# Kernel tuning notes

Measured on AMD Instinct MI355X. Metric: run time of the kernel, lower is better.

## Reference

```python
import jax, jax.numpy as jnp
import numpy as np

B, N, M, D, H = 4, 2048, 2048, 1024, 16
HD = D // H


def setup_inputs() -> dict:
    key = jax.random.key(0)
    ks = jax.random.split(key, 16)
    s = 1.0 / np.sqrt(D)
    inp = {
        "Q": jax.random.normal(ks[0], (B, N, D), jnp.float32),
        "K": jax.random.normal(ks[1], (B, M, D), jnp.float32),
        "V": jax.random.normal(ks[2], (B, M, D), jnp.float32),
        "attn_bias": jax.random.normal(ks[3], (B, N, M), jnp.float32),
        "mask": jax.random.randint(ks[4], (B, M), 0, 2).astype(bool),
        # linear params (torch nn.Linear: y = x @ W.T + b)
        "Wq": jax.random.uniform(ks[5], (D, D), jnp.float32, -s, s),
        "bq": jax.random.uniform(ks[6], (D,), jnp.float32, -s, s),
        "Wk": jax.random.uniform(ks[7], (D, D), jnp.float32, -s, s),
        "bk": jax.random.uniform(ks[8], (D,), jnp.float32, -s, s),
        "Wv": jax.random.uniform(ks[9], (D, D), jnp.float32, -s, s),
        "bv": jax.random.uniform(ks[10], (D,), jnp.float32, -s, s),
        "Wo": jax.random.uniform(ks[11], (D, D), jnp.float32, -s, s),
        "bo": jax.random.uniform(ks[12], (D,), jnp.float32, -s, s),
    }
    return inp


def reference(Q, K, V, attn_bias, mask, Wq, bq, Wk, bk, Wv, bv, Wo, bo):
    b, n, d = Q.shape
    m = K.shape[1]
    # bias (B,N,M) -> (B,1,N,M); mask (B,M) True = masked out (-inf)
    bias = attn_bias[:, None, :, :]
    bias = jnp.where(mask[:, None, None, :], -jnp.inf, bias)
    # projections, split heads: (B, H, len, head_dim)
    q = (Q @ Wq.T + bq).reshape(b, n, H, HD).transpose(0, 2, 1, 3)
    k = (K @ Wk.T + bk).reshape(b, m, H, HD).transpose(0, 2, 1, 3)
    v = (V @ Wv.T + bv).reshape(b, m, H, HD).transpose(0, 2, 1, 3)
    scale = 1.0 / np.sqrt(HD).astype(np.float32)
    attn = jnp.einsum("bhid,bhjd->bhij", q * scale, k) + bias
    attn = jax.nn.softmax(attn, axis=-1)
    out = jnp.einsum("bhij,bhjd->bhid", attn, v)
    out = out.transpose(0, 2, 1, 3).reshape(b, n, d)
    return out @ Wo.T + bo
```

## Files before the change

kernel.cpp:

```cpp
#include <hip/hip_runtime.h>
#include <hip/hip_bf16.h>

#define Bq 4
#define Nq 2048
#define Mq 2048
#define Dq 1024
#define Hq 16

typedef __attribute__((ext_vector_type(8))) short short8;
typedef __attribute__((ext_vector_type(4))) short short4v;
typedef __attribute__((ext_vector_type(4))) float floatx4;
typedef __attribute__((ext_vector_type(16))) float floatx16;
typedef __attribute__((ext_vector_type(4))) unsigned uint4v;

static __device__ __forceinline__ short f2bf(float f) {
    __hip_bfloat16 h = __float2bfloat16(f);
    short r;
    __builtin_memcpy(&r, &h, 2);
    return r;
}
static __device__ __forceinline__ float bf2f(short s) {
    unsigned u = ((unsigned)(unsigned short)s) << 16;
    float f;
    __builtin_memcpy(&f, &u, 4);
    return f;
}
static __device__ __forceinline__ unsigned cvtpk_bf16(float lo, float hi) {
    unsigned r;
    asm("v_cvt_pk_bf16_f32 %0, %1, %2" : "=v"(r) : "v"(lo), "v"(hi));
    return r;
}
static __device__ __forceinline__ void swap32(unsigned &a, unsigned &b) {
    asm("v_permlane32_swap_b32 %0, %1" : "+v"(a), "+v"(b));
}
static __device__ __forceinline__ float exp2_fast(float x) {
    float r;
    asm("v_exp_f32 %0, %1" : "=v"(r) : "v"(x));
    return r;
}
static __device__ __forceinline__ void gld16(const void* g, void* l) {
    __builtin_amdgcn_global_load_lds(
        (const __attribute__((address_space(1))) unsigned int*)g,
        (__attribute__((address_space(3))) unsigned int*)l, 16, 0, 0);
}

__global__ void bias_prep(const float* __restrict__ bias, const int* __restrict__ mask,
                          short* __restrict__ out)
{
    const long i = ((long)blockIdx.x * 256 + threadIdx.x) * 8;
    const int m = (int)(i & (Mq - 1));
    const int b = (int)(i >> 22);
    floatx4 f0 = *(const floatx4*)(bias + i);
    floatx4 f1 = *(const floatx4*)(bias + i + 4);
    const int* mp = mask + b * Mq + m;
    short8 o;
#pragma unroll
    for (int e = 0; e < 4; ++e) {
        o[e]     = mp[e]     ? f2bf(-1e38f) : f2bf(f0[e] * 1.44269504f);
        o[e + 4] = mp[e + 4] ? f2bf(-1e38f) : f2bf(f1[e] * 1.44269504f);
    }
    *(short8*)(out + i) = o;
}

__global__ void cvt_w(const float* __restrict__ w0, const float* __restrict__ w1,
                      const float* __restrict__ w2, const float* __restrict__ w3,
                      short* __restrict__ out)
{
    const int z = blockIdx.y;
    const float* s = (z == 0) ? w0 : (z == 1) ? w1 : (z == 2) ? w2 : w3;
    short* d = out + (size_t)z * (Dq * Dq);
    const int i = (blockIdx.x * 256 + threadIdx.x) * 8;
    floatx4 f0 = *(const floatx4*)(s + i);
    floatx4 f1 = *(const floatx4*)(s + i + 4);
    short8 o;
#pragma unroll
    for (int e = 0; e < 4; ++e) { o[e] = f2bf(f0[e]); o[e + 4] = f2bf(f1[e]); }
    *(short8*)(d + i) = o;
}

struct GB {
    const void* A[3];
    const short* W[3];
    const float* bias[3];
    void* C[3];
    float scale[3];
    int omode[3];
};

template<bool ABF>
__global__ __launch_bounds__(256, 3)
void gemm_bt(GB gb, int K)
{
    __shared__ __align__(16) short As[2][128 * 32];
    __shared__ __align__(16) short Bs[2][128 * 32];

    const int z = blockIdx.z;
    const char* Ap = (const char*)gb.A[z];
    const short* Wp = gb.W[z];

    const int tid = threadIdx.x;
    const int lane = tid & 63;
    const int wid = tid >> 6;
    const int wr = wid >> 1, wc = wid & 1;
    const int g = lane >> 4, c = lane & 15;
    const long row0 = (long)blockIdx.x * 128;
    const int col0 = blockIdx.y * 128;

    const int srow = tid >> 1;
    const int sk = (tid & 1) * 16;
    const int R0 = tid >> 2;
    const int ub = (tid & 3) ^ ((R0 >> 1) & 3);
    const short* bsrc = Wp + ((long)col0 + R0) * K + ub * 8;

    floatx4 acc[4][4];
#pragma unroll
    for (int i = 0; i < 4; ++i)
#pragma unroll
        for (int j = 0; j < 4; ++j) acc[i][j] = (floatx4)0.0f;

    {
        char* d0 = (char*)Bs + wid * 1024;
        gld16(bsrc, d0);
        gld16(bsrc + 64L * K, d0 + 4096);
    }
    {
        short8 a0, a1;
        if constexpr (ABF) {
            const short* ap = (const short*)Ap + (row0 + srow) * (long)K + sk;
            a0 = *(const short8*)ap; a1 = *(const short8*)(ap + 8);
        } else {
            const float* ap = (const float*)Ap + (row0 + srow) * (long)K + sk;
            floatx4 f0 = *(const floatx4*)ap,       f1 = *(const floatx4*)(ap + 4),
                    f2 = *(const floatx4*)(ap + 8), f3 = *(const floatx4*)(ap + 12);
#pragma unroll
            for (int e = 0; e < 4; ++e) {
                a0[e] = f2bf(f0[e]); a0[e + 4] = f2bf(f1[e]);
                a1[e] = f2bf(f2[e]); a1[e + 4] = f2bf(f3[e]);
            }
        }
        short8* As8 = (short8*)As;
        const int u0 = sk >> 3, sw = (srow >> 1) & 3;
        As8[srow * 4 + ((u0)     ^ sw)] = a0;
        As8[srow * 4 + ((u0 + 1) ^ sw)] = a1;
    }
    __syncthreads();

    int buf = 0;
    for (int kt = 0; kt < K; kt += 32) {
        const bool nlast = (kt + 32 < K);
        floatx4 f0, f1, f2, f3;
        short8 s0, s1;
        if (nlast) {
            char* d0 = (char*)Bs + (buf ^ 1) * 8192 + wid * 1024;
            gld16(bsrc + kt + 32, d0);
            gld16(bsrc + 64L * K + kt + 32, d0 + 4096);
            if constexpr (ABF) {
                const short* ap = (const short*)Ap + (row0 + srow) * (long)K + kt + 32 + sk;
                s0 = *(const short8*)ap; s1 = *(const short8*)(ap + 8);
            } else {
                const float* ap = (const float*)Ap + (row0 + srow) * (long)K + kt + 32 + sk;
                f0 = *(const floatx4*)ap;       f1 = *(const floatx4*)(ap + 4);
                f2 = *(const floatx4*)(ap + 8); f3 = *(const floatx4*)(ap + 12);
            }
        }
        short8* As8 = (short8*)((char*)As + buf * 8192);
        short8* Bs8 = (short8*)((char*)Bs + buf * 8192);
        short8 af[4], bfq[4];
#pragma unroll
        for (int fm = 0; fm < 4; ++fm) {
            const int r = wr * 64 + fm * 16 + c;
            af[fm] = As8[r * 4 + (g ^ ((r >> 1) & 3))];
        }
#pragma unroll
        for (int fn = 0; fn < 4; ++fn) {
            const int cc = wc * 64 + fn * 16 + c;
            bfq[fn] = Bs8[cc * 4 + (g ^ ((cc >> 1) & 3))];
        }
#pragma unroll
        for (int fm = 0; fm < 4; ++fm)
#pragma unroll
            for (int fn = 0; fn < 4; ++fn)
                acc[fm][fn] = __builtin_amdgcn_mfma_f32_16x16x32_bf16(af[fm], bfq[fn], acc[fm][fn], 0, 0, 0);
        if (nlast) {
            short8 a0, a1;
            if constexpr (ABF) { a0 = s0; a1 = s1; }
            else {
#pragma unroll
                for (int e = 0; e < 4; ++e) {
                    a0[e] = f2bf(f0[e]); a0[e + 4] = f2bf(f1[e]);
                    a1[e] = f2bf(f2[e]); a1[e + 4] = f2bf(f3[e]);
                }
            }
            short8* An8 = (short8*)((char*)As + (buf ^ 1) * 8192);
            const int u0 = sk >> 3, sw = (srow >> 1) & 3;
            An8[srow * 4 + ((u0)     ^ sw)] = a0;
            An8[srow * 4 + ((u0 + 1) ^ sw)] = a1;
        }
        __syncthreads();
        buf ^= 1;
    }

    const float sc = gb.scale[z];
    const float* bp = gb.bias[z];
    const int om = gb.omode[z];
    void* Cp = gb.C[z];
#pragma unroll
    for (int fn = 0; fn < 4; ++fn) {
        const int ccol = col0 + wc * 64 + fn * 16 + c;
        const float bv = bp[ccol];
#pragma unroll
        for (int fm = 0; fm < 4; ++fm) {
            const long r0 = row0 + wr * 64 + fm * 16 + g * 4;
#pragma unroll
            for (int reg = 0; reg < 4; ++reg) {
                const float val = (acc[fm][fn][reg] + bv) * sc;
                const long rr = r0 + reg;
                if (om == 0) {
                    ((short*)Cp)[rr * Dq + ccol] = f2bf(val);
                } else if (om == 1) {
                    const long idx = ((long)(rr >> 11) * Dq + ccol) * (long)Mq + (rr & (Mq - 1));
                    ((short*)Cp)[idx] = f2bf(val);
                } else {
                    ((float*)Cp)[rr * Dq + ccol] = val;
                }
            }
        }
    }
}

__global__ __launch_bounds__(256, 4)
void attn_fused(const short* __restrict__ qg_, const short* __restrict__ kg_,
                const short* __restrict__ vtg, const short* __restrict__ bmg,
                short* __restrict__ outg)
{
    __shared__ __align__(16) short k_lds[2][64 * 64];
    __shared__ __align__(16) short v_lds[2][64 * 64];

    const int tid = threadIdx.x;
    const int lane = tid & 63;
    const int w = tid >> 6;
    const int hi = lane >> 5;
    const int q31 = lane & 31;

    const int blk = blockIdx.x;
    const int bh = blk & 63;
    const int qt = blk >> 6;
    const int b = bh >> 4, h = bh & 15;

    const long qbase = (long)b * Nq + qt * 128 + w * 32;

    short8 qf[4];
#pragma unroll
    for (int ks = 0; ks < 4; ++ks)
        qf[ks] = *(const short8*)(qg_ + (qbase + q31) * Dq + h * 64 + ks * 16 + hi * 8);

    floatx16 oa[2];
    oa[0] = (floatx16)0.0f; oa[1] = (floatx16)0.0f;
    float m_s = -1e37f, l_s = 0.0f;

    const int sr = tid >> 3;
    const int su = (tid & 7) ^ (sr & 7);
    const char* ksrc = (const char*)(kg_ + ((long)b * Mq + sr) * Dq + h * 64 + su * 8);
    const char* vsrc = (const char*)(vtg + ((long)b * Dq + h * 64 + sr) * Mq + su * 8);

#define STAGE(bf, kt2) do {                                                   \
        const long j0b = (long)(kt2) * 64;                                    \
        char* kd = (char*)k_lds + (bf) * 8192 + w * 1024;                     \
        char* vd = (char*)v_lds + (bf) * 8192 + w * 1024;                     \
        gld16(ksrc + j0b * (Dq * 2), kd);                                     \
        gld16(ksrc + (j0b + 32) * (Dq * 2), kd + 4096);                       \
        gld16(vsrc + j0b * 2, vd);                                            \
        gld16(vsrc + 32L * Mq * 2 + j0b * 2, vd + 4096);                      \
    } while (0)

    STAGE(0, 0);
    __syncthreads();

    int buf = 0;
    for (int kt = 0; kt < 32; ++kt) {
        if (kt < 31) STAGE(buf ^ 1, kt + 1);
        const short* brow = bmg + (qbase + q31) * Mq + (long)kt * 64;
        short4v bb[8];
#pragma unroll
        for (int kg = 0; kg < 2; ++kg)
#pragma unroll
            for (int Qh = 0; Qh < 4; ++Qh)
                bb[kg * 4 + Qh] = *(const short4v*)(brow + kg * 32 + Qh * 8 + hi * 4);

        const char* kb = (const char*)k_lds + buf * 8192;
        const char* vb = (const char*)v_lds + buf * 8192;

        floatx16 sa[2];
#pragma unroll
        for (int kg = 0; kg < 2; ++kg) {
            short8 kf[4];
#pragma unroll
            for (int ks = 0; ks < 4; ++ks) {
                const int r = kg * 32 + q31;
                const int up = (2 * ks + hi) ^ (r & 7);
                kf[ks] = *(const short8*)(kb + r * 128 + up * 16);
            }
            sa[kg] = (floatx16)0.0f;
#pragma unroll
            for (int ks = 0; ks < 4; ++ks)
                sa[kg] = __builtin_amdgcn_mfma_f32_32x32x16_bf16(kf[ks], qf[ks], sa[kg], 0, 0, 0);
        }

        float p[32];
#pragma unroll
        for (int kg = 0; kg < 2; ++kg)
#pragma unroll
            for (int Qh = 0; Qh < 4; ++Qh) {
                const short4v bv4 = bb[kg * 4 + Qh];
#pragma unroll
                for (int e = 0; e < 4; ++e)
                    p[kg * 16 + Qh * 4 + e] = sa[kg][Qh * 4 + e] + bf2f(bv4[e]);
            }
        float t16[16];
#pragma unroll
        for (int i = 0; i < 16; ++i) t16[i] = fmaxf(p[2 * i], p[2 * i + 1]);
#pragma unroll
        for (int i = 0; i < 8; ++i) t16[i] = fmaxf(t16[2 * i], t16[2 * i + 1]);
        t16[0] = fmaxf(fmaxf(fmaxf(t16[0], t16[1]), fmaxf(t16[2], t16[3])),
                       fmaxf(fmaxf(t16[4], t16[5]), fmaxf(t16[6], t16[7])));
        const float pm = fmaxf(t16[0], __shfl_xor(t16[0], 32));
        if (!__all(pm <= m_s + 11.5f)) {
            const float mn = fmaxf(m_s, pm);
            const float al = exp2_fast(m_s - mn);
            l_s *= al;
            oa[0] *= al; oa[1] *= al;
            m_s = mn;
        }
#pragma unroll
        for (int i = 0; i < 32; ++i) p[i] = exp2_fast(p[i] - m_s);
        float s16[16];
#pragma unroll
        for (int i = 0; i < 16; ++i) s16[i] = p[2 * i] + p[2 * i + 1];
#pragma unroll
        for (int i = 0; i < 8; ++i) s16[i] = s16[2 * i] + s16[2 * i + 1];
        float rs = ((s16[0] + s16[1]) + (s16[2] + s16[3])) +
                   ((s16[4] + s16[5]) + (s16[6] + s16[7]));
        rs += __shfl_xor(rs, 32);
        l_s += rs;

        uint4v pw[4];
#pragma unroll
        for (int kg = 0; kg < 2; ++kg) {
            unsigned w0 = cvtpk_bf16(p[kg * 16 + 0], p[kg * 16 + 1]);
            unsigned w1 = cvtpk_bf16(p[kg * 16 + 2], p[kg * 16 + 3]);
            unsigned w2 = cvtpk_bf16(p[kg * 16 + 4], p[kg * 16 + 5]);
            unsigned w3 = cvtpk_bf16(p[kg * 16 + 6], p[kg * 16 + 7]);
            swap32(w0, w2); swap32(w1, w3);
            pw[kg * 2][0] = w0; pw[kg * 2][1] = w1; pw[kg * 2][2] = w2; pw[kg * 2][3] = w3;
            unsigned w4 = cvtpk_bf16(p[kg * 16 + 8],  p[kg * 16 + 9]);
            unsigned w5 = cvtpk_bf16(p[kg * 16 + 10], p[kg * 16 + 11]);
            unsigned w6 = cvtpk_bf16(p[kg * 16 + 12], p[kg * 16 + 13]);
            unsigned w7 = cvtpk_bf16(p[kg * 16 + 14], p[kg * 16 + 15]);
            swap32(w4, w6); swap32(w5, w7);
            pw[kg * 2 + 1][0] = w4; pw[kg * 2 + 1][1] = w5; pw[kg * 2 + 1][2] = w6; pw[kg * 2 + 1][3] = w7;
        }

#pragma unroll
        for (int dg = 0; dg < 2; ++dg) {
            short8 vf[4];
#pragma unroll
            for (int ks = 0; ks < 4; ++ks) {
                const int r = dg * 32 + q31;
                const int up = (2 * ks + hi) ^ (r & 7);
                vf[ks] = *(const short8*)(vb + r * 128 + up * 16);
            }
#pragma unroll
            for (int ks = 0; ks < 4; ++ks)
                oa[dg] = __builtin_amdgcn_mfma_f32_32x32x16_bf16(
                    vf[ks], __builtin_bit_cast(short8, pw[ks]), oa[dg], 0, 0, 0);
        }
        __syncthreads();
        buf ^= 1;
    }
#undef STAGE

    const float invl = 1.0f / l_s;
    short* op = outg + (qbase + q31) * Dq + h * 64;
#pragma unroll
    for (int dg = 0; dg < 2; ++dg)
#pragma unroll
        for (int Qh = 0; Qh < 4; ++Qh) {
            short4v t;
#pragma unroll
            for (int e = 0; e < 4; ++e)
                t[e] = f2bf(oa[dg][Qh * 4 + e] * invl);
            *(short4v*)(op + dg * 32 + Qh * 8 + hi * 4) = t;
        }
}

extern "C" void kernel_launch(void* const* d_in, const int* in_sizes, int n_in,
                              void* d_out, int out_size, void* d_ws, size_t ws_size,
                              hipStream_t stream)
{
    const float* Q    = (const float*)d_in[0];
    const float* K    = (const float*)d_in[1];
    const float* V    = (const float*)d_in[2];
    const float* bias = (const float*)d_in[3];
    const int*   mask = (const int*)d_in[4];
    const float* Wq   = (const float*)d_in[5];
    const float* bq   = (const float*)d_in[6];
    const float* Wk   = (const float*)d_in[7];
    const float* bk   = (const float*)d_in[8];
    const float* Wv   = (const float*)d_in[9];
    const float* bv   = (const float*)d_in[10];
    const float* Wo   = (const float*)d_in[11];
    const float* bo   = (const float*)d_in[12];

    const size_t TSZ = (size_t)Bq * Nq * Dq;
    short* q_ws  = (short*)d_ws;
    short* k_ws  = q_ws  + TSZ;
    short* vt_ws = k_ws  + TSZ;
    short* a_ws  = vt_ws + TSZ;
    short* bm_ws = a_ws  + TSZ;
    short* w_ws  = bm_ws + (size_t)Bq * Nq * Mq;
    (void)ws_size;

    bias_prep<<<dim3(8192), dim3(256), 0, stream>>>(bias, mask, bm_ws);
    cvt_w<<<dim3(512, 4), dim3(256), 0, stream>>>(Wq, Wk, Wv, Wo, w_ws);

    GB g1{};
    g1.A[0] = Q;  g1.A[1] = K;  g1.A[2] = V;
    g1.W[0] = w_ws; g1.W[1] = w_ws + Dq * Dq; g1.W[2] = w_ws + 2 * Dq * Dq;
    g1.bias[0] = bq; g1.bias[1] = bk; g1.bias[2] = bv;
    g1.C[0] = q_ws; g1.C[1] = k_ws; g1.C[2] = vt_ws;
    g1.scale[0] = 0.125f * 1.44269504f; g1.scale[1] = 1.0f; g1.scale[2] = 1.0f;
    g1.omode[0] = 0; g1.omode[1] = 0; g1.omode[2] = 1;
    gemm_bt<false><<<dim3(64, 8, 3), dim3(256), 0, stream>>>(g1, Dq);

    attn_fused<<<dim3(1024), dim3(256), 0, stream>>>(q_ws, k_ws, vt_ws, bm_ws, a_ws);

    GB g2{};
    g2.A[0] = a_ws;
    g2.W[0] = w_ws + 3 * Dq * Dq;
    g2.bias[0] = bo;
    g2.C[0] = d_out;
    g2.scale[0] = 1.0f;
    g2.omode[0] = 2;
    gemm_bt<true><<<dim3(64, 8, 1), dim3(256), 0, stream>>>(g2, Dq);
}
```

Measured before the change: 342.4 us.

## Pre-convert QKV inputs to bf16 and stage A via direct LDS loads

Adds a conversion pass that turns Q, K and V into bf16 in aliased workspace buffers, so the projection gemm can load both operands with direct global-to-LDS copies instead of converting fp32 in registers. bias_prep is moved after the projection to reuse the workspace. The attention kernel also initialises the score accumulator with the bias so the MFMA performs the add. This costs an extra full read and write of the inputs in exchange for a simpler, better-pipelined gemm loop.

```diff
diff --git a/kernel.cpp b/kernel.cpp
--- a/kernel.cpp
+++ b/kernel.cpp
@@ -62,14 +62,14 @@
     *(short8*)(out + i) = o;
 }
 
-__global__ void cvt_w(const float* __restrict__ w0, const float* __restrict__ w1,
-                      const float* __restrict__ w2, const float* __restrict__ w3,
-                      short* __restrict__ out)
+__global__ void cvt_bf(const float* __restrict__ s0, const float* __restrict__ s1,
+                       const float* __restrict__ s2, const float* __restrict__ s3,
+                       short* __restrict__ out, long per)
 {
     const int z = blockIdx.y;
-    const float* s = (z == 0) ? w0 : (z == 1) ? w1 : (z == 2) ? w2 : w3;
-    short* d = out + (size_t)z * (Dq * Dq);
-    const int i = (blockIdx.x * 256 + threadIdx.x) * 8;
+    const float* s = (z == 0) ? s0 : (z == 1) ? s1 : (z == 2) ? s2 : s3;
+    short* d = out + (long)z * per;
+    const long i = ((long)blockIdx.x * 256 + threadIdx.x) * 8;
     floatx4 f0 = *(const floatx4*)(s + i);
     floatx4 f1 = *(const floatx4*)(s + i + 4);
     short8 o;
@@ -79,7 +79,7 @@
 }
 
 struct GB {
-    const void* A[3];
+    const short* A[3];
     const short* W[3];
     const float* bias[3];
     void* C[3];
@@ -87,15 +87,14 @@
     int omode[3];
 };
 
-template<bool ABF>
 __global__ __launch_bounds__(256, 3)
-void gemm_bt(GB gb, int K)
+void gemm_all(GB gb, int K)
 {
     __shared__ __align__(16) short As[2][128 * 32];
     __shared__ __align__(16) short Bs[2][128 * 32];
 
     const int z = blockIdx.z;
-    const char* Ap = (const char*)gb.A[z];
+    const short* Ap = gb.A[z];
     const short* Wp = gb.W[z];
 
     const int tid = threadIdx.x;
@@ -106,10 +105,9 @@
     const long row0 = (long)blockIdx.x * 128;
     const int col0 = blockIdx.y * 128;
 
-    const int srow = tid >> 1;
-    const int sk = (tid & 1) * 16;
     const int R0 = tid >> 2;
     const int ub = (tid & 3) ^ ((R0 >> 1) & 3);
+    const short* asrc = Ap + (row0 + R0) * (long)K + ub * 8;
     const short* bsrc = Wp + ((long)col0 + R0) * K + ub * 8;
 
     floatx4 acc[4][4];
@@ -118,51 +116,21 @@
 #pragma unroll
         for (int j = 0; j < 4; ++j) acc[i][j] = (floatx4)0.0f;
 
-    {
-        char* d0 = (char*)Bs + wid * 1024;
-        gld16(bsrc, d0);
-        gld16(bsrc + 64L * K, d0 + 4096);
-    }
-    {
-        short8 a0, a1;
-        if constexpr (ABF) {
-            const short* ap = (const short*)Ap + (row0 + srow) * (long)K + sk;
-            a0 = *(const short8*)ap; a1 = *(const short8*)(ap + 8);
-        } else {
-            const float* ap = (const float*)Ap + (row0 + srow) * (long)K + sk;
-            floatx4 f0 = *(const floatx4*)ap,       f1 = *(const floatx4*)(ap + 4),
-                    f2 = *(const floatx4*)(ap + 8), f3 = *(const floatx4*)(ap + 12);
-#pragma unroll
-            for (int e = 0; e < 4; ++e) {
-                a0[e] = f2bf(f0[e]); a0[e + 4] = f2bf(f1[e]);
-                a1[e] = f2bf(f2[e]); a1[e + 4] = f2bf(f3[e]);
-            }
-        }
-        short8* As8 = (short8*)As;
-        const int u0 = sk >> 3, sw = (srow >> 1) & 3;
-        As8[srow * 4 + ((u0)     ^ sw)] = a0;
-        As8[srow * 4 + ((u0 + 1) ^ sw)] = a1;
-    }
+#define GSTAGE(buf, koff) do {                                                \
+        char* ad = (char*)As + (buf) * 8192 + wid * 1024;                     \
+        char* bd = (char*)Bs + (buf) * 8192 + wid * 1024;                     \
+        gld16(asrc + (koff), ad);                                             \
+        gld16(asrc + 64L * K + (koff), ad + 4096);                            \
+        gld16(bsrc + (koff), bd);                                             \
+        gld16(bsrc + 64L * K + (koff), bd + 4096);                            \
+    } while (0)
+
+    GSTAGE(0, 0);
     __syncthreads();
 
     int buf = 0;
     for (int kt = 0; kt < K; kt += 32) {
-        const bool nlast = (kt + 32 < K);
-        floatx4 f0, f1, f2, f3;
-        short8 s0, s1;
-        if (nlast) {
-            char* d0 = (char*)Bs + (buf ^ 1) * 8192 + wid * 1024;
-            gld16(bsrc + kt + 32, d0);
-            gld16(bsrc + 64L * K + kt + 32, d0 + 4096);
-            if constexpr (ABF) {
-                const short* ap = (const short*)Ap + (row0 + srow) * (long)K + kt + 32 + sk;
-                s0 = *(const short8*)ap; s1 = *(const short8*)(ap + 8);
-            } else {
-                const float* ap = (const float*)Ap + (row0 + srow) * (long)K + kt + 32 + sk;
-                f0 = *(const floatx4*)ap;       f1 = *(const floatx4*)(ap + 4);
-                f2 = *(const floatx4*)(ap + 8); f3 = *(const floatx4*)(ap + 12);
-            }
-        }
+        if (kt + 32 < K) GSTAGE(buf ^ 1, kt + 32);
         short8* As8 = (short8*)((char*)As + buf * 8192);
         short8* Bs8 = (short8*)((char*)Bs + buf * 8192);
         short8 af[4], bfq[4];
@@ -181,24 +149,10 @@
 #pragma unroll
             for (int fn = 0; fn < 4; ++fn)
                 acc[fm][fn] = __builtin_amdgcn_mfma_f32_16x16x32_bf16(af[fm], bfq[fn], acc[fm][fn], 0, 0, 0);
-        if (nlast) {
-            short8 a0, a1;
-            if constexpr (ABF) { a0 = s0; a1 = s1; }
-            else {
-#pragma unroll
-                for (int e = 0; e < 4; ++e) {
-                    a0[e] = f2bf(f0[e]); a0[e + 4] = f2bf(f1[e]);
-                    a1[e] = f2bf(f2[e]); a1[e + 4] = f2bf(f3[e]);
-                }
-            }
-            short8* An8 = (short8*)((char*)As + (buf ^ 1) * 8192);
-            const int u0 = sk >> 3, sw = (srow >> 1) & 3;
-            An8[srow * 4 + ((u0)     ^ sw)] = a0;
-            An8[srow * 4 + ((u0 + 1) ^ sw)] = a1;
-        }
         __syncthreads();
         buf ^= 1;
     }
+#undef GSTAGE
 
     const float sc = gb.scale[z];
     const float* bp = gb.bias[z];
@@ -292,6 +246,15 @@
 
         floatx16 sa[2];
 #pragma unroll
+        for (int kg = 0; kg < 2; ++kg)
+#pragma unroll
+            for (int Qh = 0; Qh < 4; ++Qh) {
+                const short4v b4 = bb[kg * 4 + Qh];
+#pragma unroll
+                for (int e = 0; e < 4; ++e)
+                    sa[kg][Qh * 4 + e] = bf2f(b4[e]);
+            }
+#pragma unroll
         for (int kg = 0; kg < 2; ++kg) {
             short8 kf[4];
 #pragma unroll
@@ -300,7 +263,6 @@
                 const int up = (2 * ks + hi) ^ (r & 7);
                 kf[ks] = *(const short8*)(kb + r * 128 + up * 16);
             }
-            sa[kg] = (floatx16)0.0f;
 #pragma unroll
             for (int ks = 0; ks < 4; ++ks)
                 sa[kg] = __builtin_amdgcn_mfma_f32_32x32x16_bf16(kf[ks], qf[ks], sa[kg], 0, 0, 0);
@@ -310,12 +272,8 @@
 #pragma unroll
         for (int kg = 0; kg < 2; ++kg)
 #pragma unroll
-            for (int Qh = 0; Qh < 4; ++Qh) {
-                const short4v bv4 = bb[kg * 4 + Qh];
-#pragma unroll
-                for (int e = 0; e < 4; ++e)
-                    p[kg * 16 + Qh * 4 + e] = sa[kg][Qh * 4 + e] + bf2f(bv4[e]);
-            }
+            for (int j = 0; j < 16; ++j)
+                p[kg * 16 + j] = sa[kg][j];
         float t16[16];
 #pragma unroll
         for (int i = 0; i < 16; ++i) t16[i] = fmaxf(p[2 * i], p[2 * i + 1]);
@@ -417,20 +375,25 @@
     short* vt_ws = k_ws  + TSZ;
     short* a_ws  = vt_ws + TSZ;
     short* bm_ws = a_ws  + TSZ;
-    short* w_ws  = bm_ws + (size_t)Bq * Nq * Mq;
+    short* w_ws  = bm_ws + 2 * TSZ;
+    short* qin_ws = a_ws;
+    short* kin_ws = bm_ws;
+    short* vin_ws = bm_ws + TSZ;
     (void)ws_size;
 
-    bias_prep<<<dim3(8192), dim3(256), 0, stream>>>(bias, mask, bm_ws);
-    cvt_w<<<dim3(512, 4), dim3(256), 0, stream>>>(Wq, Wk, Wv, Wo, w_ws);
+    cvt_bf<<<dim3(512, 4), dim3(256), 0, stream>>>(Wq, Wk, Wv, Wo, w_ws, (long)Dq * Dq);
+    cvt_bf<<<dim3(4096, 3), dim3(256), 0, stream>>>(Q, K, V, V, qin_ws, (long)TSZ);
 
     GB g1{};
-    g1.A[0] = Q;  g1.A[1] = K;  g1.A[2] = V;
+    g1.A[0] = qin_ws; g1.A[1] = kin_ws; g1.A[2] = vin_ws;
     g1.W[0] = w_ws; g1.W[1] = w_ws + Dq * Dq; g1.W[2] = w_ws + 2 * Dq * Dq;
     g1.bias[0] = bq; g1.bias[1] = bk; g1.bias[2] = bv;
     g1.C[0] = q_ws; g1.C[1] = k_ws; g1.C[2] = vt_ws;
     g1.scale[0] = 0.125f * 1.44269504f; g1.scale[1] = 1.0f; g1.scale[2] = 1.0f;
     g1.omode[0] = 0; g1.omode[1] = 0; g1.omode[2] = 1;
-    gemm_bt<false><<<dim3(64, 8, 3), dim3(256), 0, stream>>>(g1, Dq);
+    gemm_all<<<dim3(64, 8, 3), dim3(256), 0, stream>>>(g1, Dq);
+
+    bias_prep<<<dim3(8192), dim3(256), 0, stream>>>(bias, mask, bm_ws);
 
     attn_fused<<<dim3(1024), dim3(256), 0, stream>>>(q_ws, k_ws, vt_ws, bm_ws, a_ws);
 
@@ -441,5 +404,5 @@
     g2.C[0] = d_out;
     g2.scale[0] = 1.0f;
     g2.omode[0] = 2;
-    gemm_bt<true><<<dim3(64, 8, 1), dim3(256), 0, stream>>>(g2, Dq);
-}
+    gemm_all<<<dim3(64, 8, 1), dim3(256), 0, stream>>>(g2, Dq);
+}
```

Measured after the change: 328.3 us. 1.04x faster.
